# Kernel optimization log

Hardware: AMD Instinct MI355X
Metric: run time of the kernel (lower is better)

## Reference

```python
import jax, jax.numpy as jnp
from jax import lax
import numpy as np

DIM = 384; NH = 8; N = 16; K = 4; DIN = 768; DTR = 24  # d_model, heads, d_state, d_conv, d_inner, dt_rank
B = 8; Hh = 48; Ww = 48


def _ln(x, g, b):
    m = jnp.mean(x, -1, keepdims=True)
    v = jnp.mean((x - m) ** 2, -1, keepdims=True)
    return (x - m) / jnp.sqrt(v + 1e-5) * g + b


def _mamba(x, in_w, in_b, conv_w, conv_b, xp_w, dt_w, dt_b, A_log, Dp, out_w, out_b):
    # x: (B, L, DIM)
    Bb, L, _ = x.shape
    xz = x @ in_w.T + in_b                      # (B, L, 2*DIN)
    xm, z = xz[..., :DIN], xz[..., DIN:]
    # depthwise causal conv over sequence
    xc = jnp.pad(xm.transpose(0, 2, 1), ((0, 0), (0, 0), (K - 1, 0)))  # (B, DIN, L+K-1)
    xconv = lax.conv_general_dilated(xc, conv_w[:, None, :], (1,), 'VALID',
                                     feature_group_count=DIN,
                                     dimension_numbers=('NCH', 'OIH', 'NCH'))
    u = jax.nn.silu((xconv + conv_b[None, :, None]).transpose(0, 2, 1))  # (B, L, DIN)
    dbc = u @ xp_w.T                            # (B, L, DTR + 2N)
    delta = jax.nn.softplus(dbc[..., :DTR] @ dt_w.T + dt_b)  # (B, L, DIN)
    Bm = dbc[..., DTR:DTR + N]                  # (B, L, N)
    Cm = dbc[..., DTR + N:]                     # (B, L, N)
    A = -jnp.exp(A_log)                         # (DIN, N)

    def step(h, inp):
        d_t, B_t, C_t, u_t = inp                # (B,DIN),(B,N),(B,N),(B,DIN)
        dA = jnp.exp(d_t[:, :, None] * A)       # (B, DIN, N)
        h = h * dA + d_t[:, :, None] * B_t[:, None, :] * u_t[:, :, None]
        y = jnp.einsum('bdn,bn->bd', h, C_t)
        return h, y

    h0 = jnp.zeros((Bb, DIN, N), x.dtype)
    xs = (delta.transpose(1, 0, 2), Bm.transpose(1, 0, 2), Cm.transpose(1, 0, 2), u.transpose(1, 0, 2))
    _, ys = lax.scan(step, h0, xs)
    y = ys.transpose(1, 0, 2) + u * Dp
    y = y * jax.nn.silu(z)
    return y @ out_w.T + out_b


def _forward(x, n1_g, n1_b, ap_w, ap_b, n2_g, n2_b, in_w, in_b, conv_w, conv_b, xp_w, dt_w, dt_b,
             A_log, Dp, out_w, out_b, mod_w1, mod_b1, mod_w2, mod_b2, n3_g, n3_b,
             fc1_w, fc1_b, fc2_w, fc2_b):
    Bb, C, Hc, Wc = x.shape
    xs = x.reshape(Bb, C, Hc * Wc).transpose(0, 2, 1)          # (B, L, C)
    xn = _ln(xs, n1_g, n1_b)
    attn = jax.nn.softmax(xn @ ap_w.T + ap_b, axis=1)          # softmax over sequence
    gc = jnp.einsum('bln,blc->bnc', attn, xn).mean(1)          # (B, C)
    mod = jax.nn.silu(gc @ mod_w1.T + mod_b1) @ mod_w2.T + mod_b2
    xn2 = _ln(xs, n2_g, n2_b)
    mo = _mamba(xn2, in_w, in_b, conv_w, conv_b, xp_w, dt_w, dt_b, A_log, Dp, out_w, out_b)
    mo = mo * (1.0 + mod[:, None, :])
    xs = xs + mo
    h = _ln(xs, n3_g, n3_b)
    h = jax.nn.gelu(h @ fc1_w.T + fc1_b) @ fc2_w.T + fc2_b
    xs = xs + h
    return xs.transpose(0, 2, 1).reshape(Bb, C, Hc, Wc)


def setup_inputs() -> dict:
    key = jax.random.key(0)
    ks = jax.random.split(key, 16)
    s = 0.02
    p = {}
    p['x'] = jax.random.normal(ks[0], (B, DIM, Hh, Ww), jnp.float32)
    p['n1_g'] = jnp.ones((DIM,), jnp.float32); p['n1_b'] = jnp.zeros((DIM,), jnp.float32)
    p['ap_w'] = jax.random.normal(ks[1], (NH, DIM), jnp.float32) * s; p['ap_b'] = jnp.zeros((NH,), jnp.float32)
    p['n2_g'] = jnp.ones((DIM,), jnp.float32); p['n2_b'] = jnp.zeros((DIM,), jnp.float32)
    p['in_w'] = jax.random.normal(ks[2], (2 * DIN, DIM), jnp.float32) * s; p['in_b'] = jnp.zeros((2 * DIN,), jnp.float32)
    p['conv_w'] = jax.random.normal(ks[3], (DIN, K), jnp.float32) * s; p['conv_b'] = jnp.zeros((DIN,), jnp.float32)
    p['xp_w'] = jax.random.normal(ks[4], (DTR + 2 * N, DIN), jnp.float32) * s
    p['dt_w'] = jax.random.normal(ks[5], (DIN, DTR), jnp.float32) * s
    p['dt_b'] = jax.random.uniform(ks[6], (DIN,), jnp.float32, minval=-4.0, maxval=-2.0)
    p['A_log'] = jnp.log(jnp.tile(jnp.arange(1, N + 1, dtype=jnp.float32), (DIN, 1)))
    p['Dp'] = jnp.ones((DIN,), jnp.float32)
    p['out_w'] = jax.random.normal(ks[7], (DIM, DIN), jnp.float32) * s; p['out_b'] = jnp.zeros((DIM,), jnp.float32)
    p['mod_w1'] = jax.random.normal(ks[8], (2 * DIM, DIM), jnp.float32) * s; p['mod_b1'] = jnp.zeros((2 * DIM,), jnp.float32)
    p['mod_w2'] = jax.random.normal(ks[9], (DIM, 2 * DIM), jnp.float32) * s; p['mod_b2'] = jnp.zeros((DIM,), jnp.float32)
    p['n3_g'] = jnp.ones((DIM,), jnp.float32); p['n3_b'] = jnp.zeros((DIM,), jnp.float32)
    p['fc1_w'] = jax.random.normal(ks[10], (4 * DIM, DIM), jnp.float32) * s; p['fc1_b'] = jnp.zeros((4 * DIM,), jnp.float32)
    p['fc2_w'] = jax.random.normal(ks[11], (DIM, 4 * DIM), jnp.float32) * s; p['fc2_b'] = jnp.zeros((DIM,), jnp.float32)
    return p


def reference(x, n1_g, n1_b, ap_w, ap_b, n2_g, n2_b, in_w, in_b, conv_w, conv_b, xp_w, dt_w, dt_b,
              A_log, Dp, out_w, out_b, mod_w1, mod_b1, mod_w2, mod_b2, n3_g, n3_b,
              fc1_w, fc1_b, fc2_w, fc2_b):
    return _forward(x, n1_g, n1_b, ap_w, ap_b, n2_g, n2_b, in_w, in_b, conv_w, conv_b, xp_w,
                    dt_w, dt_b, A_log, Dp, out_w, out_b, mod_w1, mod_b1, mod_w2, mod_b2,
                    n3_g, n3_b, fc1_w, fc1_b, fc2_w, fc2_b)
```

## Files before the change

kernel.cpp:

```cpp
#include <hip/hip_runtime.h>
#include <math.h>

#define DIMC 384
#define NHD 8
#define NSTATE 16
#define DINN 768
#define DTRK 24
#define BB 8
#define LSEQ 2304
#define MROWS (BB*LSEQ)
#define NCH 64
#define TCH 36
#define L2E 1.44269504f

typedef unsigned short u16;
typedef short bf16x8 __attribute__((ext_vector_type(8)));
typedef float f32x4 __attribute__((ext_vector_type(4)));

__device__ __forceinline__ float sigmoid_(float x){ return 1.f/(1.f+__expf(-x)); }
__device__ __forceinline__ float silu_(float x){ return x*sigmoid_(x); }
__device__ __forceinline__ float softplus_(float x){ return (x>20.f)?x:log1pf(__expf(x)); }
__device__ __forceinline__ float gelu_(float x){
  float x3=x*x*x;
  return 0.5f*x*(1.f+tanhf(0.7978845608028654f*(x+0.044715f*x3)));
}
__device__ __forceinline__ float bfu2f(u16 u){
  union{unsigned int i; float f;} c; c.i=((unsigned int)u)<<16; return c.f;
}
__device__ __forceinline__ u16 f2bfu(float f){
  union{float f; unsigned int i;} c; c.f=f;
  unsigned int r = c.i + 0x7FFFu + ((c.i>>16)&1u);
  return (u16)(r>>16);
}
__device__ __forceinline__ void gl_lds16(const u16* g, u16* l){
  __builtin_amdgcn_global_load_lds((__attribute__((address_space(1))) void*)g,
      (__attribute__((address_space(3))) void*)l, 16, 0, 0);
}

__device__ __forceinline__ u16 swzw(const float* __restrict__ s, int o, int KT,
                                    int Nsrc, int Ksrc){
  int e = o&7, l = (o>>3)&63, rest = o>>9;
  int kt = rest % KT, nt = rest / KT;
  int n = nt*16 + (l&15);
  int k = kt*32 + ((l>>4)<<3) + e;
  return (n<Nsrc && k<Ksrc) ? f2bfu(s[(size_t)n*Ksrc + k]) : (u16)0;
}

#define O1 589824
#define O2 688128
#define O3 983040
#define O4 1572864
#define O5 2162688
#define O6 2187264
#define OEND 2190336
__global__ void k_cvtall(const float* __restrict__ inw, const float* __restrict__ xpw,
    const float* __restrict__ outw, const float* __restrict__ fc1w,
    const float* __restrict__ fc2w, const float* __restrict__ dtw,
    u16* __restrict__ inw_b, u16* __restrict__ xpw_pad, u16* __restrict__ outw_b,
    u16* __restrict__ fc1w_b, u16* __restrict__ fc2w_b, u16* __restrict__ dtw_pad,
    float* __restrict__ gc){
  int i = blockIdx.x*256+threadIdx.x;
  if(i >= OEND) return;
  if(i < O1){ inw_b[i]   = swzw(inw,  i,    12, 1536, 384); }
  else if(i < O2){ xpw_pad[i-O1] = swzw(xpw,  i-O1, 24, 56,   768); }
  else if(i < O3){ outw_b[i-O2]  = swzw(outw, i-O2, 24, 384,  768); }
  else if(i < O4){ fc1w_b[i-O3]  = swzw(fc1w, i-O3, 12, 1536, 384); }
  else if(i < O5){ fc2w_b[i-O4]  = swzw(fc2w, i-O4, 48, 384,  1536); }
  else if(i < O6){ dtw_pad[i-O5] = swzw(dtw,  i-O5, 1,  768,  24); }
  else { gc[i-O6]=0.f; }
}

__global__ void k_transpose(const float* __restrict__ x, float* __restrict__ xs){
  __shared__ float tile[32][33];
  int b = blockIdx.z;
  int t0 = blockIdx.x*32, c0 = blockIdx.y*32;
  int tx = threadIdx.x, ty = threadIdx.y;
  const float* xb = x + (size_t)b*DIMC*LSEQ;
  #pragma unroll
  for(int q=0;q<4;q++)
    tile[ty+q*8][tx] = xb[(size_t)(c0+ty+q*8)*LSEQ + t0+tx];
  __syncthreads();
  float* xsb = xs + (size_t)b*LSEQ*DIMC;
  #pragma unroll
  for(int q=0;q<4;q++)
    xsb[(size_t)(t0+ty+q*8)*DIMC + c0+tx] = tile[tx][ty+q*8];
}

__global__ __launch_bounds__(64) void k_lnstats(const float* __restrict__ xs,
   const float* __restrict__ g1,const float* __restrict__ b1,
   const float* __restrict__ g2,const float* __restrict__ b2,
   const float* __restrict__ apw,const float* __restrict__ apb,
   float* __restrict__ meanr, float* __restrict__ rstdr,
   u16* __restrict__ xn2, float* __restrict__ scores){
  int row = blockIdx.x;
  int lane = threadIdx.x;
  const float* xr = xs + (size_t)row*DIMC;
  float v[6];
  float s=0.f, s2=0.f;
  #pragma unroll
  for(int i=0;i<6;i++){ v[i]=xr[lane+i*64]; s+=v[i]; s2+=v[i]*v[i]; }
  #pragma unroll
  for(int m=32;m>=1;m>>=1){ s += __shfl_xor(s,m); s2 += __shfl_xor(s2,m); }
  float mean = s*(1.f/DIMC);
  float var  = s2*(1.f/DIMC)-mean*mean;
  float rstd = rsqrtf(var+1e-5f);
  if(lane==0){ meanr[row]=mean; rstdr[row]=rstd; }
  float xv1[6];
  #pragma unroll
  for(int i=0;i<6;i++){
    int c = lane+i*64;
    float nx = (v[i]-mean)*rstd;
    xv1[i] = nx*g1[c]+b1[c];
    xn2[(size_t)row*DIMC+c] = f2bfu(nx*g2[c]+b2[c]);
  }
  #pragma unroll
  for(int h=0;h<NHD;h++){
    float p=0.f;
    #pragma unroll
    for(int i=0;i<6;i++) p += xv1[i]*apw[h*DIMC+lane+i*64];
    #pragma unroll
    for(int m=32;m>=1;m>>=1) p += __shfl_xor(p,m);
    if(lane==0) scores[(size_t)row*NHD+h]=p+apb[h];
  }
}

__global__ __launch_bounds__(256) void k_softmax_L(float* __restrict__ sc){
  int bh = blockIdx.x; int b = bh>>3, h = bh&7;
  int tid = threadIdx.x;
  __shared__ float red[8];
  const size_t base = (size_t)b*LSEQ*NHD + h;
  float mx = -1e30f;
  for(int l=tid;l<LSEQ;l+=256) mx = fmaxf(mx, sc[base + (size_t)l*NHD]);
  #pragma unroll
  for(int m=32;m>=1;m>>=1) mx = fmaxf(mx, __shfl_xor(mx,m));
  if((tid&63)==0) red[tid>>6]=mx;
  __syncthreads();
  mx = fmaxf(fmaxf(red[0],red[1]),fmaxf(red[2],red[3]));
  float sum=0.f;
  for(int l=tid;l<LSEQ;l+=256) sum += __expf(sc[base+(size_t)l*NHD]-mx);
  #pragma unroll
  for(int m=32;m>=1;m>>=1) sum += __shfl_xor(sum,m);
  if((tid&63)==0) red[4+(tid>>6)]=sum;
  __syncthreads();
  float inv = 1.f/(red[4]+red[5]+red[6]+red[7]);
  for(int l=tid;l<LSEQ;l+=256){
    size_t idx = base+(size_t)l*NHD;
    sc[idx] = __expf(sc[idx]-mx)*inv;
  }
}

__global__ __launch_bounds__(384) void k_gc(const float* __restrict__ attn,
    const float* __restrict__ xs, const float* __restrict__ meanr,
    const float* __restrict__ rstdr, const float* __restrict__ g1,
    const float* __restrict__ b1, float* __restrict__ gc){
  int b = blockIdx.x; int chunk = blockIdx.y; int c = threadIdx.x;
  int l0 = chunk*48;
  float acc=0.f, accw=0.f;
  for(int l=0;l<48;l++){
    int row = b*LSEQ + l0+l;
    const float* a = attn + (size_t)row*NHD;
    float ww = (((a[0]+a[1])+(a[2]+a[3]))+((a[4]+a[5])+(a[6]+a[7])))*0.125f;
    acc  += ww*(xs[(size_t)row*DIMC+c]-meanr[row])*rstdr[row];
    accw += ww;
  }
  atomicAdd(&gc[b*DIMC+c], acc*g1[c]+accw*b1[c]);
}

__global__ __launch_bounds__(256) void k_mod1(const float* __restrict__ gc,
    const float* __restrict__ w1, const float* __restrict__ b1,
    float* __restrict__ modh){
  int b = blockIdx.x; int n = blockIdx.y*64 + (threadIdx.x>>2);
  int sub = threadIdx.x&3;
  const float4* g = (const float4*)(gc + b*DIMC) + sub*24;
  const float4* wr = (const float4*)(w1 + (size_t)n*DIMC) + sub*24;
  float acc=0.f;
  #pragma unroll
  for(int k=0;k<24;k++){
    float4 a=g[k], w=wr[k];
    acc += a.x*w.x + a.y*w.y + a.z*w.z + a.w*w.w;
  }
  acc += __shfl_xor(acc,1); acc += __shfl_xor(acc,2);
  if(sub==0) modh[b*768+n] = silu_(acc+b1[n]);
}
__global__ __launch_bounds__(256) void k_mod2(const float* __restrict__ modh,
    const float* __restrict__ w2, const float* __restrict__ b2,
    float* __restrict__ mod){
  int b = blockIdx.x; int n = blockIdx.y*64 + (threadIdx.x>>2);
  int sub = threadIdx.x&3;
  const float4* g = (const float4*)(modh + b*768) + sub*48;
  const float4* wr = (const float4*)(w2 + (size_t)n*768) + sub*48;
  float acc=0.f;
  #pragma unroll
  for(int k=0;k<48;k++){
    float4 a=g[k], w=wr[k];
    acc += a.x*w.x + a.y*w.y + a.z*w.z + a.w*w.w;
  }
  acc += __shfl_xor(acc,1); acc += __shfl_xor(acc,2);
  if(sub==0) mod[b*DIMC+n] = acc+b2[n];
}

template<int EPI>
__device__ __forceinline__ void mg_epilogue(
    f32x4 (&acc)[4][4], int m0, int n0, int wr, int wc, int lrow, int lk,
    const float* bias, void* outp, int N, const float* aux, void* outp2)
{
  #pragma unroll
  for(int i=0;i<4;i++){
    int row = m0 + wr*64 + i*16 + lk*4;
    #pragma unroll
    for(int j=0;j<4;j++){
      int col = n0 + wc*64 + j*16 + lrow;
      float bc = bias ? bias[col] : 0.f;
      f32x4 v = acc[i][j];
      if(EPI==0){
        u16* o = (u16*)outp;
        #pragma unroll
        for(int r=0;r<4;r++) o[(size_t)(row+r)*N + col] = f2bfu(v[r]+bc);
      } else if(EPI==1){
        u16* o = (u16*)outp;
        #pragma unroll
        for(int r=0;r<4;r++) o[(size_t)(row+r)*N + col] = f2bfu(gelu_(v[r]+bc));
      } else if(EPI==2){
        float* o = (float*)outp;
        int bi = row/LSEQ;
        float sc = 1.f + aux[bi*DIMC + col];
        #pragma unroll
        for(int r=0;r<4;r++) o[(size_t)(row+r)*DIMC + col] += (v[r]+bc)*sc;
      } else if(EPI==3){
        float* o = (float*)outp;
        int bi = row/LSEQ, t = row - bi*LSEQ;
        float4 s;
        s.x = aux[(size_t)(row+0)*DIMC+col] + v[0] + bc;
        s.y = aux[(size_t)(row+1)*DIMC+col] + v[1] + bc;
        s.z = aux[(size_t)(row+2)*DIMC+col] + v[2] + bc;
        s.w = aux[(size_t)(row+3)*DIMC+col] + v[3] + bc;
        *reinterpret_cast<float4*>(&o[((size_t)(bi*DIMC+col))*LSEQ + t]) = s;
      } else if(EPI==4){
        float* o = (float*)outp;
        if(col < N){
          #pragma unroll
          for(int r=0;r<4;r++) o[(size_t)(row+r)*N + col] = v[r]+bc;
        }
      } else if(EPI==5){
        u16* o = (col < 768) ? (u16*)outp : (u16*)outp2;
        int cc = (col < 768) ? col : col - 768;
        #pragma unroll
        for(int r=0;r<4;r++) o[(size_t)(row+r)*768 + cc] = f2bfu(v[r]+bc);
      } else {
        u16* o = (u16*)outp;
        #pragma unroll
        for(int r=0;r<4;r++) o[(size_t)(row+r)*N + col] = f2bfu(softplus_(v[r]+bc));
      }
    }
  }
}

#define MG_STEP(KT_I, CUR, BIN, BOUT, VMSTR)                                   \
  {                                                                            \
    if((KT_I)+1 < KT){                                                         \
      _Pragma("unroll")                                                        \
      for(int j=0;j<4;j++)                                                     \
        BOUT[j] = *reinterpret_cast<const bf16x8*>(wp + 512 + j*(KTTOT*512));  \
    }                                                                          \
    asm volatile("s_waitcnt " VMSTR ::: "memory");                             \
    __builtin_amdgcn_s_barrier();                                              \
    bf16x8 af[4];                                                              \
    {                                                                          \
      const u16* lbase = &lA[CUR][lofs];                                       \
      _Pragma("unroll")                                                        \
      for(int i=0;i<4;i++)                                                     \
        af[i] = *reinterpret_cast<const bf16x8*>(lbase + i*128);               \
    }                                                                          \
    asm volatile("s_waitcnt lgkmcnt(0)" ::: "memory");                         \
    __builtin_amdgcn_s_barrier();                                              \
    if((KT_I)+2 < KT){                                                         \
      gl_lds16(Ag0 + ((KT_I)+2)*32,      (CUR)? ld1 : ld0);                    \
      gl_lds16(Ag0 + ((KT_I)+2)*32 + 16, (CUR)? hd1 : hd0);                    \
    }                                                                          \
    _Pragma("unroll")                                                          \
    for(int i=0;i<4;i++)                                                       \
      _Pragma("unroll")                                                        \
      for(int j=0;j<4;j++)                                                     \
        acc[i][j] = __builtin_amdgcn_mfma_f32_16x16x32_bf16(af[i], BIN[j],     \
                                                            acc[i][j], 0,0,0);\
    wp += 512;                                                                 \
  }

template<int EPI, int KLOOP, int KSTRIDE = KLOOP>
__global__ __launch_bounds__(256,4) void k_mgemm(
    const u16* __restrict__ A, const u16* __restrict__ Wf,
    const float* __restrict__ bias, void* __restrict__ outp,
    int N, const float* __restrict__ aux, void* __restrict__ outp2)
{
  constexpr int KT = KLOOP/32;
  constexpr int KTTOT = KSTRIDE/32;
  __shared__ u16 lA[2][4096];
  int tid = threadIdx.x;
  int m0 = blockIdx.x*128, n0 = blockIdx.y*128;
  int wid = tid>>6, lane = tid&63;
  int wr = wid>>1, wc = wid&1;
  int lrow = lane&15, lk = lane>>4;
  f32x4 acc[4][4];
  #pragma unroll
  for(int i=0;i<4;i++)
    #pragma unroll
    for(int j=0;j<4;j++){ acc[i][j][0]=0.f; acc[i][j][1]=0.f; acc[i][j][2]=0.f; acc[i][j][3]=0.f; }

  int r0 = tid & 127, k0 = tid >> 7;
  size_t zofsA = 0, zofsW = 0;
  if(KSTRIDE != KLOOP){
    zofsA = (size_t)blockIdx.z * KLOOP;
    zofsW = (size_t)blockIdx.z * KT * 512;
    outp  = (float*)outp + (size_t)blockIdx.z * MROWS * N;
  }
  const u16* Ag0 = A + (size_t)(m0+r0)*KSTRIDE + zofsA + k0*8;
  const u16* wp  = Wf + ((size_t)((n0>>4) + wc*4)*KTTOT)*512 + zofsW + (size_t)lane*8;
  const int lofs = (lk*128 + wr*64 + lrow)*8;
  u16* ld0 = &lA[0][tid*8];  u16* hd0 = &lA[0][2048+tid*8];
  u16* ld1 = &lA[1][tid*8];  u16* hd1 = &lA[1][2048+tid*8];

  gl_lds16(Ag0,    ld0);
  gl_lds16(Ag0+16, hd0);
  if(KT>1){
    gl_lds16(Ag0+32, ld1);
    gl_lds16(Ag0+48, hd1);
  }
  bf16x8 bA[4], bB[4];
  #pragma unroll
  for(int j=0;j<4;j++) bA[j] = *reinterpret_cast<const bf16x8*>(wp + j*(KTTOT*512));

  if(KT==1){
    MG_STEP(0, 0, bA, bB, "vmcnt(0)")
  } else {
    MG_STEP(0, 0, bA, bB, "vmcnt(4)")
    for(int kt=1; kt<KT-1; kt+=2){
      MG_STEP(kt,   1, bB, bA, "vmcnt(6)")
      MG_STEP(kt+1, 0, bA, bB, "vmcnt(6)")
    }
    MG_STEP(KT-1, 1, bB, bA, "vmcnt(0)")
  }

  mg_epilogue<EPI>(acc, m0, n0, wr, wc, lrow, lk, bias, outp, N, aux, outp2);
}

__global__ void k_xpred(const float* __restrict__ P, float* __restrict__ dbc,
                        u16* __restrict__ dt32){
  int idx = blockIdx.x*256+threadIdx.x;
  if(idx >= MROWS*56) return;
  int row = idx/56, c = idx - row*56;
  float s = P[idx] + P[idx + (size_t)MROWS*56] + P[idx + (size_t)2*MROWS*56]
          + P[idx + (size_t)3*MROWS*56];
  dbc[idx] = s;
  if(c < DTRK) dt32[(size_t)row*32 + c] = f2bfu(s);
  if(c < 8)    dt32[(size_t)row*32 + DTRK + c] = 0;
}

__global__ void k_conv(const u16* __restrict__ xm, const float* __restrict__ cw,
                       const float* __restrict__ cb, u16* __restrict__ u){
  int idx = blockIdx.x*256+threadIdx.x;
  if(idx >= MROWS*(DINN/8)) return;
  int j = idx % (DINN/8); int r = idx / (DINN/8);
  int t = r % LSEQ; int d0 = j*8;
  float4 w4_[8];
  #pragma unroll
  for(int e=0;e<8;e++) w4_[e] = reinterpret_cast<const float4*>(cw)[d0+e];
  float acc[8];
  #pragma unroll
  for(int e=0;e<8;e++) acc[e]=cb[d0+e];
  #pragma unroll
  for(int k=0;k<4;k++){
    int tt=t+k-3;
    if(tt>=0){
      uint4 v = *reinterpret_cast<const uint4*>(&xm[(size_t)(r+k-3)*DINN + d0]);
      unsigned vv[4]={v.x,v.y,v.z,v.w};
      #pragma unroll
      for(int e=0;e<8;e++){
        u16 raw = (e&1)? (u16)(vv[e>>1]>>16) : (u16)(vv[e>>1]&0xffffu);
        float wk = (k==0)? w4_[e].x : (k==1)? w4_[e].y : (k==2)? w4_[e].z : w4_[e].w;
        acc[e] += bfu2f(raw)*wk;
      }
    }
  }
  u16 outv[8];
  #pragma unroll
  for(int e=0;e<8;e++) outv[e]=f2bfu(silu_(acc[e]));
  *reinterpret_cast<uint4*>(&u[(size_t)r*DINN+d0]) = *reinterpret_cast<const uint4*>(outv);
}

__global__ __launch_bounds__(256) void k_scan1(
  const u16* __restrict__ dt_, const u16* __restrict__ u_,
  const float* __restrict__ dbc, const float* __restrict__ alog,
  float* __restrict__ ssum, float* __restrict__ hloc)
{
  __shared__ float Bsh[TCH][16];
  int bid = blockIdx.x;
  int b = bid/(NCH*3); int rem = bid%(NCH*3); int ch = rem/3; int dblk = rem%3;
  int tid = threadIdx.x; int d = dblk*256 + tid;
  size_t rbase = (size_t)b*LSEQ + (size_t)ch*TCH;
  for(int j=tid; j<TCH*16; j+=256){
    int row=j>>4, n=j&15;
    Bsh[row][n] = dbc[(rbase+row)*56 + DTRK + n];
  }
  float Acl2[16];
  float a0 = -__expf(alog[(size_t)d*16])*L2E;
  bool fast = true;
  #pragma unroll
  for(int n=0;n<16;n++){
    Acl2[n] = -__expf(alog[(size_t)d*16+n])*L2E;
    float tgt = (float)(n+1)*a0;
    fast = fast && (fabsf(Acl2[n]-tgt) <= 1e-4f*fabsf(tgt));
  }
  float h[16];
  #pragma unroll
  for(int n=0;n<16;n++) h[n]=0.f;
  float S=0.f;
  const u16* dtp = dt_ + rbase*DINN + d;
  const u16* up  = u_  + rbase*DINN + d;
  __syncthreads();
  if(fast){
    for(int t=0;t<TCH;t++){
      float dt = bfu2f(dtp[(size_t)t*DINN]);
      float uv = bfu2f(up[(size_t)t*DINN]);
      float G = dt*uv;
      S += dt;
      float e = exp2f(dt*a0), w = e;
      const float4* b4 = (const float4*)Bsh[t];
      float4 B0=b4[0],B1=b4[1],B2=b4[2],B3=b4[3];
      float Bv[16]={B0.x,B0.y,B0.z,B0.w,B1.x,B1.y,B1.z,B1.w,
                    B2.x,B2.y,B2.z,B2.w,B3.x,B3.y,B3.z,B3.w};
      #pragma unroll
      for(int n=0;n<16;n++){ h[n] = h[n]*w + G*Bv[n]; w *= e; }
    }
  } else {
    for(int t=0;t<TCH;t++){
      float dt = bfu2f(dtp[(size_t)t*DINN]);
      float uv = bfu2f(up[(size_t)t*DINN]);
      float G = dt*uv;
      S += dt;
      const float4* b4 = (const float4*)Bsh[t];
      float4 B0=b4[0],B1=b4[1],B2=b4[2],B3=b4[3];
      float Bv[16]={B0.x,B0.y,B0.z,B0.w,B1.x,B1.y,B1.z,B1.w,
                    B2.x,B2.y,B2.z,B2.w,B3.x,B3.y,B3.z,B3.w};
      #pragma unroll
      for(int n=0;n<16;n++) h[n] = h[n]*exp2f(dt*Acl2[n]) + G*Bv[n];
    }
  }
  ssum[((size_t)b*NCH+ch)*DINN + d] = S;
  float* hp = hloc + (((size_t)b*NCH+ch)*DINN + d)*16;
  #pragma unroll
  for(int n=0;n<16;n++) hp[n] = h[n];
}

__global__ __launch_bounds__(256) void k_scan2(
  const float* __restrict__ ssum, const float* __restrict__ alog,
  float* __restrict__ hl)
{
  int gid = blockIdx.x*256+threadIdx.x;
  int n = gid & 15; int d = (gid>>4)%DINN; int b = gid/(DINN*NSTATE);
  float Acl2 = -__expf(alog[(size_t)d*16+n])*L2E;
  float hin=0.f;
  for(int ch=0; ch<NCH; ch++){
    size_t sidx = ((size_t)b*NCH+ch)*DINN + d;
    size_t idx  = sidx*16 + n;
    float a = exp2f(ssum[sidx]*Acl2);
    float hold = hl[idx];
    hl[idx] = hin;
    hin = a*hin + hold;
  }
}

__global__ __launch_bounds__(256) void k_scan3(
  const u16* __restrict__ dt_, u16* uy, const u16* __restrict__ z_,
  const float* __restrict__ dbc, const float* __restrict__ alog,
  const float* __restrict__ Dp, const float* __restrict__ hin)
{
  __shared__ float BC[TCH][32];
  int bid = blockIdx.x;
  int b = bid/(NCH*3); int rem = bid%(NCH*3); int ch = rem/3; int dblk = rem%3;
  int tid = threadIdx.x; int d = dblk*256 + tid;
  size_t rbase = (size_t)b*LSEQ + (size_t)ch*TCH;
  for(int j=tid; j<TCH*32; j+=256){
    int row=j>>5, c=j&31;
    BC[row][c] = dbc[(rbase+row)*56 + DTRK + c];
  }
  float Acl2[16], h[16];
  const float* hp = hin + (((size_t)b*NCH+ch)*DINN + d)*16;
  float a0 = -__expf(alog[(size_t)d*16])*L2E;
  bool fast = true;
  #pragma unroll
  for(int n=0;n<16;n++){
    Acl2[n] = -__expf(alog[(size_t)d*16+n])*L2E;
    float tgt = (float)(n+1)*a0;
    fast = fast && (fabsf(Acl2[n]-tgt) <= 1e-4f*fabsf(tgt));
    h[n] = hp[n];
  }
  float Dv = Dp[d];
  const u16* dtp = dt_ + rbase*DINN + d;
  u16*       uyp = uy  + rbase*DINN + d;
  const u16* zp  = z_  + rbase*DINN + d;
  __syncthreads();
  if(fast){
    for(int t=0;t<TCH;t++){
      float dt = bfu2f(dtp[(size_t)t*DINN]);
      float uv = bfu2f(uyp[(size_t)t*DINN]);
      float zv = bfu2f(zp[(size_t)t*DINN]);
      float G = dt*uv;
      float e = exp2f(dt*a0), w = e;
      const float4* bc4 = (const float4*)BC[t];
      float4 B0=bc4[0],B1=bc4[1],B2=bc4[2],B3=bc4[3];
      float4 C0=bc4[4],C1=bc4[5],C2=bc4[6],C3=bc4[7];
      float Bv[16]={B0.x,B0.y,B0.z,B0.w,B1.x,B1.y,B1.z,B1.w,
                    B2.x,B2.y,B2.z,B2.w,B3.x,B3.y,B3.z,B3.w};
      float Cv[16]={C0.x,C0.y,C0.z,C0.w,C1.x,C1.y,C1.z,C1.w,
                    C2.x,C2.y,C2.z,C2.w,C3.x,C3.y,C3.z,C3.w};
      float y0=0.f,y1=0.f,y2=0.f,y3=0.f;
      #pragma unroll
      for(int n=0;n<16;n++){
        h[n] = h[n]*w + G*Bv[n];
        w *= e;
        if((n&3)==0) y0 += h[n]*Cv[n];
        else if((n&3)==1) y1 += h[n]*Cv[n];
        else if((n&3)==2) y2 += h[n]*Cv[n];
        else y3 += h[n]*Cv[n];
      }
      float y = (y0+y1)+(y2+y3);
      uyp[(size_t)t*DINN] = f2bfu((y + uv*Dv)*silu_(zv));
    }
  } else {
    for(int t=0;t<TCH;t++){
      float dt = bfu2f(dtp[(size_t)t*DINN]);
      float uv = bfu2f(uyp[(size_t)t*DINN]);
      float zv = bfu2f(zp[(size_t)t*DINN]);
      float G = dt*uv;
      const float4* bc4 = (const float4*)BC[t];
      float4 B0=bc4[0],B1=bc4[1],B2=bc4[2],B3=bc4[3];
      float4 C0=bc4[4],C1=bc4[5],C2=bc4[6],C3=bc4[7];
      float Bv[16]={B0.x,B0.y,B0.z,B0.w,B1.x,B1.y,B1.z,B1.w,
                    B2.x,B2.y,B2.z,B2.w,B3.x,B3.y,B3.z,B3.w};
      float Cv[16]={C0.x,C0.y,C0.z,C0.w,C1.x,C1.y,C1.z,C1.w,
                    C2.x,C2.y,C2.z,C2.w,C3.x,C3.y,C3.z,C3.w};
      float y0=0.f,y1=0.f,y2=0.f,y3=0.f;
      #pragma unroll
      for(int n=0;n<16;n++){
        h[n] = h[n]*exp2f(dt*Acl2[n]) + G*Bv[n];
        if((n&3)==0) y0 += h[n]*Cv[n];
        else if((n&3)==1) y1 += h[n]*Cv[n];
        else if((n&3)==2) y2 += h[n]*Cv[n];
        else y3 += h[n]*Cv[n];
      }
      float y = (y0+y1)+(y2+y3);
      uyp[(size_t)t*DINN] = f2bfu((y + uv*Dv)*silu_(zv));
    }
  }
}

__global__ __launch_bounds__(64) void k_ln3(const float* __restrict__ xin,
    const float* __restrict__ g, const float* __restrict__ bb, u16* __restrict__ xout){
  int row = blockIdx.x;
  int lane = threadIdx.x;
  const float* xr = xin + (size_t)row*DIMC;
  float v[6];
  float s=0.f, s2=0.f;
  #pragma unroll
  for(int i=0;i<6;i++){ v[i]=xr[lane+i*64]; s+=v[i]; s2+=v[i]*v[i]; }
  #pragma unroll
  for(int m=32;m>=1;m>>=1){ s += __shfl_xor(s,m); s2 += __shfl_xor(s2,m); }
  float mean = s*(1.f/DIMC);
  float var  = s2*(1.f/DIMC)-mean*mean;
  float rstd = rsqrtf(var+1e-5f);
  #pragma unroll
  for(int i=0;i<6;i++){
    int c = lane+i*64;
    xout[(size_t)row*DIMC+c] = f2bfu((v[i]-mean)*rstd*g[c]+bb[c]);
  }
}

extern "C" void kernel_launch(void* const* d_in, const int* in_sizes, int n_in,
                              void* d_out, int out_size, void* d_ws, size_t ws_size,
                              hipStream_t stream)
{
  const float* x     = (const float*)d_in[0];
  const float* n1g   = (const float*)d_in[1];
  const float* n1b   = (const float*)d_in[2];
  const float* apw   = (const float*)d_in[3];
  const float* apb   = (const float*)d_in[4];
  const float* n2g   = (const float*)d_in[5];
  const float* n2b   = (const float*)d_in[6];
  const float* inw   = (const float*)d_in[7];
  const float* inb   = (const float*)d_in[8];
  const float* convw = (const float*)d_in[9];
  const float* convb = (const float*)d_in[10];
  const float* xpw   = (const float*)d_in[11];
  const float* dtw   = (const float*)d_in[12];
  const float* dtb   = (const float*)d_in[13];
  const float* Alog  = (const float*)d_in[14];
  const float* Dp    = (const float*)d_in[15];
  const float* outw  = (const float*)d_in[16];
  const float* outb  = (const float*)d_in[17];
  const float* modw1 = (const float*)d_in[18];
  const float* modb1 = (const float*)d_in[19];
  const float* modw2 = (const float*)d_in[20];
  const float* modb2 = (const float*)d_in[21];
  const float* n3g   = (const float*)d_in[22];
  const float* n3b   = (const float*)d_in[23];
  const float* fc1w  = (const float*)d_in[24];
  const float* fc1b  = (const float*)d_in[25];
  const float* fc2w  = (const float*)d_in[26];
  const float* fc2b  = (const float*)d_in[27];

  float* ws = (float*)d_ws;
  float* XS    = ws;
  float* R1    = ws + 7077888;
  u16*   XMb   = (u16*)R1;
  u16*   DTb   = (u16*)R1;
  float* SSUM  = R1 + 7077888;
  float* HL    = R1 + 7471104;
  float* XPP   = HL;
  u16*   F1b   = (u16*)R1;
  u16*   Zb    = (u16*)(ws + 21233664);
  float* DBC   = ws + 28311552;
  float* WB    = ws + 29343744;
  u16*   inw_b   = (u16*)WB;
  u16*   xpw_pad = inw_b + 589824;
  u16*   outw_b  = xpw_pad + 98304;
  u16*   fc1w_b  = outw_b + 294912;
  u16*   fc2w_b  = fc1w_b + 589824;
  float* SCORES= ws + 30425088;
  float* MEANR = ws + 30590976;
  float* RSTDR = ws + 30609408;
  float* GC    = ws + 30627840;
  float* MODH  = ws + 30630912;
  float* MOD   = ws + 30637056;
  u16*   DT32b = (u16*)(ws + 30640128);
  u16*   dtw_pad=(u16*)(ws + 30935040);
  (void)ws_size; (void)n_in; (void)in_sizes; (void)out_size;

  u16* XN2b = (u16*)d_out;
  u16* Ub   = (u16*)d_out;
  u16* Hb   = (u16*)d_out;

  k_cvtall<<<(OEND+255)/256, 256, 0, stream>>>(inw, xpw, outw, fc1w, fc2w, dtw,
      inw_b, xpw_pad, outw_b, fc1w_b, fc2w_b, dtw_pad, GC);

  k_transpose<<<dim3(72,12,8), dim3(32,8), 0, stream>>>(x, XS);
  k_lnstats<<<MROWS, 64, 0, stream>>>(XS, n1g,n1b,n2g,n2b, apw,apb, MEANR, RSTDR, XN2b, SCORES);
  k_softmax_L<<<BB*NHD, 256, 0, stream>>>(SCORES);
  k_gc<<<dim3(BB,48), 384, 0, stream>>>(SCORES, XS, MEANR, RSTDR, n1g, n1b, GC);
  k_mod1<<<dim3(BB,12), 256, 0, stream>>>(GC, modw1, modb1, MODH);
  k_mod2<<<dim3(BB,6), 256, 0, stream>>>(MODH, modw2, modb2, MOD);

  k_mgemm<5,384><<<dim3(144,12), 256, 0, stream>>>(XN2b, inw_b, inb, XMb, 1536, nullptr, Zb);
  k_conv<<<(MROWS*(DINN/8)+255)/256, 256, 0, stream>>>(XMb, convw, convb, Ub);
  k_mgemm<4,192,768><<<dim3(144,1,4), 256, 0, stream>>>(Ub, xpw_pad, nullptr, XPP, 56, nullptr, nullptr);
  k_xpred<<<(MROWS*56+255)/256, 256, 0, stream>>>(XPP, DBC, DT32b);
  k_mgemm<7,32><<<dim3(144,6), 256, 0, stream>>>(DT32b, dtw_pad, dtb, DTb, 768, nullptr, nullptr);
  k_scan1<<<BB*NCH*3, 256, 0, stream>>>(DTb, Ub, DBC, Alog, SSUM, HL);
  k_scan2<<<384, 256, 0, stream>>>(SSUM, Alog, HL);
  k_scan3<<<BB*NCH*3, 256, 0, stream>>>(DTb, Ub, Zb, DBC, Alog, Dp, HL);
  k_mgemm<2,768><<<dim3(144,3), 256, 0, stream>>>(Ub, outw_b, outb, XS, 384, MOD, nullptr);
  k_ln3<<<MROWS, 64, 0, stream>>>(XS, n3g, n3b, Hb);
  k_mgemm<1,384><<<dim3(144,12), 256, 0, stream>>>(Hb, fc1w_b, fc1b, F1b, 1536, nullptr, nullptr);
  k_mgemm<3,1536><<<dim3(144,3), 256, 0, stream>>>(F1b, fc2w_b, fc2b, d_out, 384, XS, nullptr);
}
```

Measured before the change: 492.4 us.

## Use single-wave 64x64 direct-load GEMM with XCD swizzle for in_proj and fc1

Adds a one-wavefront GEMM kernel that computes a 64x64 output tile per block. It loads A and pre-swizzled weight fragments straight from global memory into registers with no LDS staging, and remaps block indices across the eight XCDs. This replaces the 256-thread LDS-pipelined GEMM for the two K=384, N=1536 projections, trading shared-memory reuse and explicit load pipelining for more, smaller blocks with less synchronisation. It risks more redundant global and L2 traffic, since each wave re-reads its A rows for every N tile.

```diff
diff --git a/kernel.cpp b/kernel.cpp
--- a/kernel.cpp
+++ b/kernel.cpp
@@ -341,6 +341,50 @@
   }
 
   mg_epilogue<EPI>(acc, m0, n0, wr, wc, lrow, lk, bias, outp, N, aux, outp2);
+}
+
+template<int EPI, int KLOOP>
+__global__ __launch_bounds__(64) void k_wgemm(
+    const u16* __restrict__ A, const u16* __restrict__ Wf,
+    const float* __restrict__ bias, void* __restrict__ outp,
+    int N, const float* __restrict__ aux, void* __restrict__ outp2,
+    int ntiles)
+{
+  constexpr int KT = KLOOP/32;
+  int nb = gridDim.x;
+  int chunk = nb >> 3;
+  int bid = blockIdx.x;
+  int swz = (bid & 7)*chunk + (bid >> 3);
+  int mt = swz / ntiles, nt = swz - mt*ntiles;
+  int m0 = mt*64, n0 = nt*64;
+  int lane = threadIdx.x;
+  int lrow = lane&15, lk = lane>>4;
+  f32x4 acc[4][4];
+  #pragma unroll
+  for(int i=0;i<4;i++)
+    #pragma unroll
+    for(int j=0;j<4;j++){ acc[i][j][0]=0.f; acc[i][j][1]=0.f; acc[i][j][2]=0.f; acc[i][j][3]=0.f; }
+
+  const u16* Ab = A + (size_t)(m0+lrow)*KLOOP + (size_t)lk*8;
+  const u16* wp = Wf + ((size_t)(nt*4)*KT)*512 + (size_t)lane*8;
+
+  #pragma unroll 2
+  for(int kt=0; kt<KT; kt++){
+    bf16x8 af[4], bfr[4];
+    #pragma unroll
+    for(int i=0;i<4;i++)
+      af[i] = *reinterpret_cast<const bf16x8*>(Ab + (size_t)i*16*KLOOP + kt*32);
+    #pragma unroll
+    for(int j=0;j<4;j++)
+      bfr[j] = *reinterpret_cast<const bf16x8*>(wp + ((size_t)j*KT + kt)*512);
+    #pragma unroll
+    for(int i=0;i<4;i++)
+      #pragma unroll
+      for(int j=0;j<4;j++)
+        acc[i][j] = __builtin_amdgcn_mfma_f32_16x16x32_bf16(af[i], bfr[j], acc[i][j], 0,0,0);
+  }
+
+  mg_epilogue<EPI>(acc, m0, n0, 0, 0, lrow, lk, bias, outp, N, aux, outp2);
 }
 
 __global__ void k_xpred(const float* __restrict__ P, float* __restrict__ dbc,
@@ -649,7 +693,7 @@
   k_mod1<<<dim3(BB,12), 256, 0, stream>>>(GC, modw1, modb1, MODH);
   k_mod2<<<dim3(BB,6), 256, 0, stream>>>(MODH, modw2, modb2, MOD);
 
-  k_mgemm<5,384><<<dim3(144,12), 256, 0, stream>>>(XN2b, inw_b, inb, XMb, 1536, nullptr, Zb);
+  k_wgemm<5,384><<<dim3(288*24), 64, 0, stream>>>(XN2b, inw_b, inb, XMb, 1536, nullptr, Zb, 24);
   k_conv<<<(MROWS*(DINN/8)+255)/256, 256, 0, stream>>>(XMb, convw, convb, Ub);
   k_mgemm<4,192,768><<<dim3(144,1,4), 256, 0, stream>>>(Ub, xpw_pad, nullptr, XPP, 56, nullptr, nullptr);
   k_xpred<<<(MROWS*56+255)/256, 256, 0, stream>>>(XPP, DBC, DT32b);
@@ -659,6 +703,6 @@
   k_scan3<<<BB*NCH*3, 256, 0, stream>>>(DTb, Ub, Zb, DBC, Alog, Dp, HL);
   k_mgemm<2,768><<<dim3(144,3), 256, 0, stream>>>(Ub, outw_b, outb, XS, 384, MOD, nullptr);
   k_ln3<<<MROWS, 64, 0, stream>>>(XS, n3g, n3b, Hb);
-  k_mgemm<1,384><<<dim3(144,12), 256, 0, stream>>>(Hb, fc1w_b, fc1b, F1b, 1536, nullptr, nullptr);
+  k_wgemm<1,384><<<dim3(288*24), 64, 0, stream>>>(Hb, fc1w_b, fc1b, F1b, 1536, nullptr, nullptr, 24);
   k_mgemm<3,1536><<<dim3(144,3), 256, 0, stream>>>(F1b, fc2w_b, fc2b, d_out, 384, XS, nullptr);
 }
```

New measurement: 528.1 us. 1.07x slower.
